# Kernel optimization log

Hardware: AMD Instinct MI355X
Metric: run time of the kernel (lower is better)

## Reference

```python
import jax, jax.numpy as jnp
import numpy as np

TAU = 2.0       # LIF membrane time constant (spikingjelly default)
ALPHA = 2.0     # ATan surrogate sharpness
EPS = 1e-5      # BN eps
NUM_HEADS = 12
PATCH = 2
LENTH = 256     # (H/PATCH)*(W/PATCH)

@jax.custom_vjp
def heaviside(x):
    return (x >= 0.0).astype(x.dtype)

def _hv_fwd(x):
    return heaviside(x), x

def _hv_bwd(x, g):
    sg = ALPHA / 2.0 / (1.0 + (jnp.pi / 2.0 * ALPHA * x) ** 2)  # ATan surrogate
    return (g * sg,)

heaviside.defvjp(_hv_fwd, _hv_bwd)

def lif(x):
    # multi-step LIF over leading time axis, hard reset, v_th = 1.0
    def step(v, xt):
        v = v + (xt - v) / TAU
        s = heaviside(v - 1.0)
        return v * (1.0 - s), s
    _, s = jax.lax.scan(step, jnp.zeros_like(x[0]), x)
    return s

def setup_inputs() -> dict:
    key = jax.random.key(0)
    ks = jax.random.split(key, 9)
    T, B, C, H, W = 4, 4, 384, 32, 32
    x = jax.random.normal(ks[0], (T, B, C, H, W), dtype=jnp.float32)
    Wconv = jax.random.normal(ks[1], (2 * C, C, PATCH, PATCH), dtype=jnp.float32) * (1.0 / np.sqrt(C * PATCH * PATCH))
    gamma1 = jax.random.uniform(ks[2], (2 * C,), dtype=jnp.float32, minval=0.5, maxval=1.5)
    beta1 = jax.random.normal(ks[3], (2 * C,), dtype=jnp.float32) * 0.1
    Wproj = jax.random.normal(ks[4], (C, C), dtype=jnp.float32) * (1.0 / np.sqrt(C))
    gamma2 = jax.random.uniform(ks[5], (C,), dtype=jnp.float32, minval=0.5, maxval=1.5)
    beta2 = jax.random.normal(ks[6], (C,), dtype=jnp.float32) * 0.1
    firing_rate_x = jax.random.uniform(ks[7], (1, 1, NUM_HEADS, 1, 1), dtype=jnp.float32, minval=0.05, maxval=0.5)
    firing_rate_attn = jax.random.uniform(ks[8], (1, 1, NUM_HEADS, 1, 1), dtype=jnp.float32, minval=0.05, maxval=0.5)
    return {"x": x, "Wconv": Wconv, "gamma1": gamma1, "beta1": beta1, "Wproj": Wproj,
            "gamma2": gamma2, "beta2": beta2, "firing_rate_x": firing_rate_x,
            "firing_rate_attn": firing_rate_attn}

def reference(x, Wconv, gamma1, beta1, Wproj, gamma2, beta2, firing_rate_x, firing_rate_attn):
    T, B, C, H, W = x.shape
    d = C // NUM_HEADS
    xs = lif(x)                                          # spikes [T,B,C,H,W]
    # patch conv dim -> 2*dim, stride = kernel = PATCH (eval BN: running mean 0, var 1)
    y = jax.lax.conv_general_dilated(xs.reshape(T * B, C, H, W), Wconv,
                                     (PATCH, PATCH), 'VALID',
                                     dimension_numbers=('NCHW', 'OIHW', 'NCHW'))
    bn1 = gamma1 / jnp.sqrt(1.0 + EPS)
    y = y * bn1[None, :, None, None] + beta1[None, :, None, None]
    Np = (H // PATCH) * (W // PATCH)                     # == LENTH
    y = y.reshape(T, B, NUM_HEADS, 2 * d, Np)
    y1, y2 = y[:, :, :, :d, :], y[:, :, :, d:, :]
    xr = xs.reshape(T, B, NUM_HEADS, d, H * W)
    scale1 = 1.0 / jnp.sqrt(firing_rate_x * d)
    attn = jnp.einsum('tbhdn,tbhdm->tbhnm', y1, xr) * scale1   # [T,B,h,Np,HW]
    attn = lif(attn)
    scale2 = 1.0 / jnp.sqrt(firing_rate_attn * LENTH)
    out = jnp.einsum('tbhdn,tbhnm->tbhdm', y2, attn) * scale2  # [T,B,h,d,HW]
    out = out.reshape(T, B, C, H, W)
    out = lif(out)
    out = jnp.einsum('oc,tbchw->tbohw', Wproj, out)            # 1x1 conv proj
    bn2 = gamma2 / jnp.sqrt(1.0 + EPS)
    out = out * bn2[None, None, :, None, None] + beta2[None, None, :, None, None]
    return out + x
```

## Files before the change

### kernel.cpp

```cpp
#include <hip/hip_runtime.h>
#include <hip/hip_bf16.h>
#include <math.h>


typedef __attribute__((ext_vector_type(8))) short short8;
typedef __attribute__((ext_vector_type(4))) float f32x4;

#define T_ 4
#define B_ 4
#define C_ 384
#define HW 1024
#define NH_ 12
#define Np_ 256
#define EPS_ 1e-5f
#define LDK 56

static __device__ __forceinline__ unsigned short f2bf(float f) {
    __hip_bfloat16 h = __float2bfloat16(f);
    return *reinterpret_cast<unsigned short*>(&h);
}
static __device__ __forceinline__ float bf2f(unsigned short u) {
    __hip_bfloat16 h = *reinterpret_cast<__hip_bfloat16*>(&u);
    return __bfloat162float(h);
}
static __device__ __forceinline__ void split3(float w, unsigned short& u0,
                                              unsigned short& u1, unsigned short& u2) {
    u0 = f2bf(w);  float f0 = bf2f(u0);
    float r1 = w - f0;
    u1 = f2bf(r1); float f1 = bf2f(u1);
    u2 = f2bf(r1 - f1);
}

__global__ __launch_bounds__(256) void k_wsplit(const float* __restrict__ Wc,
                                                const float* __restrict__ Wp,
                                                unsigned short* __restrict__ Wc3,
                                                unsigned short* __restrict__ Wp3) {
    const int NC = 768 * 1536;
    const int NP = 384 * 384;
    int i = blockIdx.x * 256 + threadIdx.x;
    float w; unsigned short* dst; int idx, plane;
    if (i < NC) { w = Wc[i]; dst = Wc3; idx = i; plane = NC; }
    else {
        int j = i - NC;
        if (j >= NP) return;
        w = Wp[j]; dst = Wp3; idx = j; plane = NP;
    }
    unsigned short u0, u1, u2;
    split3(w, u0, u1, u2);
    dst[idx] = u0; dst[plane + idx] = u1; dst[2 * plane + idx] = u2;
}

__global__ __launch_bounds__(256) void k_lif_im2col(const float* __restrict__ x,
                                                    unsigned short* __restrict__ Bc,
                                                    unsigned short* __restrict__ xsb) {
    int gt = blockIdx.x * 256 + threadIdx.x;
    int pw = gt & 15, ph = (gt >> 4) & 15;
    int v = gt >> 8;
    int c = v % 384, b = v / 384;
    float v00 = 0.f, v01 = 0.f, v10 = 0.f, v11 = 0.f;
    const size_t xrow = ((size_t)b * C_ + c) * HW + (size_t)(2 * ph) * 32 + 2 * pw;
#pragma unroll
    for (int t = 0; t < T_; ++t) {
        const float* px = x + (size_t)t * (B_ * C_ * HW) + xrow;
        float2 r0 = *(const float2*)px;
        float2 r1 = *(const float2*)(px + 32);
        v00 += (r0.x - v00) * 0.5f;
        v01 += (r0.y - v01) * 0.5f;
        v10 += (r1.x - v10) * 0.5f;
        v11 += (r1.y - v11) * 0.5f;
        ushort4 s;
        s.x = (v00 >= 1.f) ? 0x3F80 : 0; if (v00 >= 1.f) v00 = 0.f;
        s.y = (v01 >= 1.f) ? 0x3F80 : 0; if (v01 >= 1.f) v01 = 0.f;
        s.z = (v10 >= 1.f) ? 0x3F80 : 0; if (v10 >= 1.f) v10 = 0.f;
        s.w = (v11 >= 1.f) ? 0x3F80 : 0; if (v11 >= 1.f) v11 = 0.f;
        int tb = t * B_ + b;
        int n = tb * 256 + ph * 16 + pw;
        *(ushort4*)(Bc + (size_t)n * 1536 + 4 * c) = s;
        size_t xo = ((size_t)tb * C_ + c) * HW + (size_t)(2 * ph) * 32 + 2 * pw;
        ushort2 w0 = {s.x, s.y}, w1 = {s.z, s.w};
        *(ushort2*)(xsb + xo) = w0;
        *(ushort2*)(xsb + xo + 32) = w1;
    }
}

__global__ __launch_bounds__(256) void k_mconv(const unsigned short* __restrict__ Bc,
                                               const unsigned short* __restrict__ Wc3,
                                               const float* __restrict__ g1,
                                               const float* __restrict__ b1,
                                               const float* __restrict__ frx,
                                               const float* __restrict__ fra,
                                               unsigned short* __restrict__ y1s,
                                               unsigned short* __restrict__ y2s) {
    __shared__ short As[3][64][LDK];
    __shared__ short Bs[128][LDK];
    const int nb = blockIdx.x, mb = blockIdx.y;
    const int tid = threadIdx.x;
    const int lane = tid & 63, wave = tid >> 6;
    const int wm = wave >> 1, wn = wave & 1;
    const int quad = lane >> 4, lr = lane & 15;
    const int arow = tid >> 2, akoff = (tid & 3) * 8;
    f32x4 acc[2][4];
#pragma unroll
    for (int im = 0; im < 2; ++im)
#pragma unroll
        for (int in = 0; in < 4; ++in)
            acc[im][in] = (f32x4){0.f, 0.f, 0.f, 0.f};

    for (int k0 = 0; k0 < 1536; k0 += 32) {
#pragma unroll
        for (int s = 0; s < 3; ++s) {
            short8 a = *(const short8*)(Wc3 + ((size_t)(s * 768 + mb * 64 + arow)) * 1536 + k0 + akoff);
            *(short8*)&As[s][arow][akoff] = a;
        }
#pragma unroll
        for (int i = 0; i < 2; ++i) {
            int f = i * 256 + tid;
            int row = f >> 2, koff = (f & 3) * 8;
            short8 bv = *(const short8*)(Bc + ((size_t)(nb * 128 + row)) * 1536 + k0 + koff);
            *(short8*)&Bs[row][koff] = bv;
        }
        __syncthreads();
        short8 bf[4], af[3][2];
#pragma unroll
        for (int in = 0; in < 4; ++in)
            bf[in] = *(const short8*)&Bs[wn * 64 + in * 16 + lr][quad * 8];
#pragma unroll
        for (int s = 0; s < 3; ++s)
#pragma unroll
            for (int im = 0; im < 2; ++im)
                af[s][im] = *(const short8*)&As[s][wm * 32 + im * 16 + lr][quad * 8];
#pragma unroll
        for (int s = 0; s < 3; ++s)
#pragma unroll
            for (int im = 0; im < 2; ++im)
#pragma unroll
                for (int in = 0; in < 4; ++in)
                    acc[im][in] = __builtin_amdgcn_mfma_f32_16x16x32_bf16(af[s][im], bf[in], acc[im][in], 0, 0, 0);
        __syncthreads();
    }
    const float rs = 1.0f / sqrtf(1.0f + EPS_);
    const int h = mb;
    const float scl = (wm == 0) ? (1.0f / sqrtf(frx[h] * 32.0f))
                                : (1.0f / sqrtf(fra[h] * 256.0f));
    unsigned short* dst = (wm == 0) ? y1s : y2s;
#pragma unroll
    for (int im = 0; im < 2; ++im) {
#pragma unroll
        for (int in = 0; in < 4; ++in) {
            int n_g = nb * 128 + wn * 64 + in * 16 + lr;
            int tb = n_g >> 8, pn = n_g & 255;
            size_t base = (size_t)(tb * NH_ + h) * 3 * 8192;
            ushort4 o0, o1, o2;
#pragma unroll
            for (int r = 0; r < 4; ++r) {
                int oc = mb * 64 + wm * 32 + im * 16 + quad * 4 + r;
                float val = (acc[im][in][r] * (g1[oc] * rs) + b1[oc]) * scl;
                unsigned short u0, u1, u2;
                split3(val, u0, u1, u2);
                ((unsigned short*)&o0)[r] = u0;
                ((unsigned short*)&o1)[r] = u1;
                ((unsigned short*)&o2)[r] = u2;
            }
            int dd = im * 16 + quad * 4;
            if (wm == 0) {
                *(ushort4*)&dst[base + 0 * 8192 + (size_t)pn * 32 + dd] = o0;
                *(ushort4*)&dst[base + 1 * 8192 + (size_t)pn * 32 + dd] = o1;
                *(ushort4*)&dst[base + 2 * 8192 + (size_t)pn * 32 + dd] = o2;
            } else {
#pragma unroll
                for (int r = 0; r < 4; ++r) {
                    dst[base + 0 * 8192 + (size_t)(dd + r) * 256 + pn] = ((unsigned short*)&o0)[r];
                    dst[base + 1 * 8192 + (size_t)(dd + r) * 256 + pn] = ((unsigned short*)&o1)[r];
                    dst[base + 2 * 8192 + (size_t)(dd + r) * 256 + pn] = ((unsigned short*)&o2)[r];
                }
            }
        }
    }
}

__global__ __launch_bounds__(256) void k_attn2(const unsigned short* __restrict__ xsb,
                                               const unsigned short* __restrict__ y1s,
                                               const unsigned short* __restrict__ y2s,
                                               unsigned short* __restrict__ obt) {
    __shared__ unsigned short xb[32][40];
    __shared__ unsigned short pb[32][264];
    const int mt0 = blockIdx.x * 32;
    const int h = blockIdx.y;
    const int b = blockIdx.z;
    const int tid = threadIdx.x;
    const int lane = tid & 63, wv = tid >> 6;
    const int quad = lane >> 4, lr = lane & 15;
    const int dt = wv >> 1, ct = wv & 1;

    float vat[4][2][4];
#pragma unroll
    for (int it = 0; it < 4; ++it)
#pragma unroll
        for (int jt = 0; jt < 2; ++jt)
#pragma unroll
            for (int r = 0; r < 4; ++r) vat[it][jt][r] = 0.f;
    float vo[4] = {0.f, 0.f, 0.f, 0.f};

    for (int t = 0; t < T_; ++t) {
        const int tb = t * B_ + b;
#pragma unroll
        for (int i = 0; i < 4; ++i) {
            int e = tid + i * 256;
            int d = e >> 5, j = e & 31;
            xb[j][d] = xsb[((size_t)tb * C_ + h * 32 + d) * HW + mt0 + j];
        }
        __syncthreads();

        short8 bx[2];
#pragma unroll
        for (int jt = 0; jt < 2; ++jt)
            bx[jt] = *(const short8*)&xb[jt * 16 + lr][quad * 8];

        f32x4 acc[4][2];
#pragma unroll
        for (int it = 0; it < 4; ++it)
#pragma unroll
            for (int jt = 0; jt < 2; ++jt)
                acc[it][jt] = (f32x4){0.f, 0.f, 0.f, 0.f};

        const unsigned short* y1p = y1s + (size_t)(tb * NH_ + h) * 3 * 8192
                                        + (size_t)(wv * 64 + lr) * 32 + quad * 8;
#pragma unroll
        for (int s = 0; s < 3; ++s)
#pragma unroll
            for (int it = 0; it < 4; ++it) {
                short8 a = *(const short8*)(y1p + s * 8192 + it * 512);
#pragma unroll
                for (int jt = 0; jt < 2; ++jt)
                    acc[it][jt] = __builtin_amdgcn_mfma_f32_16x16x32_bf16(a, bx[jt], acc[it][jt], 0, 0, 0);
            }

#pragma unroll
        for (int it = 0; it < 4; ++it)
#pragma unroll
            for (int jt = 0; jt < 2; ++jt) {
                ushort4 sp;
#pragma unroll
                for (int r = 0; r < 4; ++r) {
                    float v = vat[it][jt][r];
                    v += (acc[it][jt][r] - v) * 0.5f;
                    bool s = (v >= 1.0f);
                    ((unsigned short*)&sp)[r] = s ? 0x3F80 : 0;
                    vat[it][jt][r] = s ? 0.f : v;
                }
                *(ushort4*)&pb[jt * 16 + lr][wv * 64 + it * 16 + quad * 4] = sp;
            }
        __syncthreads();

        f32x4 acc2 = (f32x4){0.f, 0.f, 0.f, 0.f};
        const unsigned short* y2p = y2s + (size_t)(tb * NH_ + h) * 3 * 8192
                                        + (size_t)(dt * 16 + lr) * 256 + quad * 8;
#pragma unroll
        for (int s = 0; s < 3; ++s)
#pragma unroll
            for (int k0 = 0; k0 < 256; k0 += 32) {
                short8 a2 = *(const short8*)(y2p + s * 8192 + k0);
                short8 b2 = *(const short8*)&pb[ct * 16 + lr][k0 + quad * 8];
                acc2 = __builtin_amdgcn_mfma_f32_16x16x32_bf16(a2, b2, acc2, 0, 0, 0);
            }

        ushort4 ob;
#pragma unroll
        for (int r = 0; r < 4; ++r) {
            float v = vo[r];
            v += (acc2[r] - v) * 0.5f;
            bool s = (v >= 1.0f);
            ((unsigned short*)&ob)[r] = s ? 0x3F80 : 0;
            vo[r] = s ? 0.f : v;
        }
        *(ushort4*)(obt + ((size_t)tb * HW + mt0 + ct * 16 + lr) * C_
                        + h * 32 + dt * 16 + quad * 4) = ob;
        __syncthreads();
    }
}

__global__ __launch_bounds__(256) void k_mproj(const unsigned short* __restrict__ obt,
                                               const unsigned short* __restrict__ Wp3,
                                               const float* __restrict__ g2,
                                               const float* __restrict__ b2,
                                               const float* __restrict__ x,
                                               float* __restrict__ out) {
    __shared__ short As[3][64][LDK];
    __shared__ short Bs[128][LDK];
    const int nb = blockIdx.x, mb = blockIdx.y;
    const int tid = threadIdx.x;
    const int lane = tid & 63, wave = tid >> 6;
    const int wm = wave >> 1, wn = wave & 1;
    const int quad = lane >> 4, lr = lane & 15;
    const int arow = tid >> 2, akoff = (tid & 3) * 8;
    f32x4 acc[2][4];
#pragma unroll
    for (int im = 0; im < 2; ++im)
#pragma unroll
        for (int in = 0; in < 4; ++in)
            acc[im][in] = (f32x4){0.f, 0.f, 0.f, 0.f};

    for (int k0 = 0; k0 < 384; k0 += 32) {
#pragma unroll
        for (int s = 0; s < 3; ++s) {
            short8 a = *(const short8*)(Wp3 + ((size_t)(s * 384 + mb * 64 + arow)) * 384 + k0 + akoff);
            *(short8*)&As[s][arow][akoff] = a;
        }
#pragma unroll
        for (int i = 0; i < 2; ++i) {
            int f = i * 256 + tid;
            int row = f >> 2, koff = (f & 3) * 8;
            short8 bv = *(const short8*)(obt + ((size_t)(nb * 128 + row)) * 384 + k0 + koff);
            *(short8*)&Bs[row][koff] = bv;
        }
        __syncthreads();
        short8 bf[4], af[3][2];
#pragma unroll
        for (int in = 0; in < 4; ++in)
            bf[in] = *(const short8*)&Bs[wn * 64 + in * 16 + lr][quad * 8];
#pragma unroll
        for (int s = 0; s < 3; ++s)
#pragma unroll
            for (int im = 0; im < 2; ++im)
                af[s][im] = *(const short8*)&As[s][wm * 32 + im * 16 + lr][quad * 8];
#pragma unroll
        for (int s = 0; s < 3; ++s)
#pragma unroll
            for (int im = 0; im < 2; ++im)
#pragma unroll
                for (int in = 0; in < 4; ++in)
                    acc[im][in] = __builtin_amdgcn_mfma_f32_16x16x32_bf16(af[s][im], bf[in], acc[im][in], 0, 0, 0);
        __syncthreads();
    }
    const float rs = 1.0f / sqrtf(1.0f + EPS_);
#pragma unroll
    for (int im = 0; im < 2; ++im) {
#pragma unroll
        for (int in = 0; in < 4; ++in) {
            int n_g = nb * 128 + wn * 64 + in * 16 + lr;
            int tb = n_g >> 10, hw = n_g & 1023;
#pragma unroll
            for (int r = 0; r < 4; ++r) {
                int o = mb * 64 + wm * 32 + im * 16 + quad * 4 + r;
                size_t idx = ((size_t)tb * C_ + o) * HW + hw;
                out[idx] = acc[im][in][r] * (g2[o] * rs) + b2[o] + x[idx];
            }
        }
    }
}

extern "C" void kernel_launch(void* const* d_in, const int* in_sizes, int n_in,
                              void* d_out, int out_size, void* d_ws, size_t ws_size,
                              hipStream_t stream) {
    const float* x      = (const float*)d_in[0];
    const float* Wconv  = (const float*)d_in[1];
    const float* gamma1 = (const float*)d_in[2];
    const float* beta1  = (const float*)d_in[3];
    const float* Wproj  = (const float*)d_in[4];
    const float* gamma2 = (const float*)d_in[5];
    const float* beta2  = (const float*)d_in[6];
    const float* frx    = (const float*)d_in[7];
    const float* fra    = (const float*)d_in[8];
    float* out = (float*)d_out;

    unsigned short* ws16 = (unsigned short*)d_ws;
    unsigned short* Bc  = ws16;
    unsigned short* obt = ws16;
    unsigned short* Wc3 = ws16 + 6291456;
    unsigned short* Wp3 = ws16 + 9830400;
    unsigned short* xsb = ws16 + 10272768;
    unsigned short* y1s = ws16 + 16564224;
    unsigned short* y2s = ws16 + 21282816;

    k_wsplit<<<5184, 256, 0, stream>>>(Wconv, Wproj, Wc3, Wp3);
    k_lif_im2col<<<1536, 256, 0, stream>>>(x, Bc, xsb);
    k_mconv<<<dim3(32, 12), 256, 0, stream>>>(Bc, Wc3, gamma1, beta1, frx, fra, y1s, y2s);
    k_attn2<<<dim3(32, 12, 4), 256, 0, stream>>>(xsb, y1s, y2s, obt);
    k_mproj<<<dim3(128, 6), 256, 0, stream>>>(obt, Wp3, gamma2, beta2, x, out);
}
```

Before: 275.4 us.

## Preload all timesteps of x, double-buffer spike tile, hoist y1/y2 fragment loads

The attention kernel now loads the x tile for all four timesteps into shared memory once at kernel start. It issues every y1 and y2 global fragment load at the top of each timestep, ahead of the MFMAs. The spike tile is double-buffered by timestep parity, so the trailing barrier per timestep is removed. The aim is to hide global-load latency behind MFMA work and cut barrier count. The cost is many more live registers (36 short8 fragments), which could lower occupancy or spill despite the launch bound of 2.

```diff
diff --git a/kernel.cpp b/kernel.cpp
--- a/kernel.cpp
+++ b/kernel.cpp
@@ -178,12 +178,12 @@
     }
 }
 
-__global__ __launch_bounds__(256) void k_attn2(const unsigned short* __restrict__ xsb,
-                                               const unsigned short* __restrict__ y1s,
-                                               const unsigned short* __restrict__ y2s,
-                                               unsigned short* __restrict__ obt) {
-    __shared__ unsigned short xb[32][40];
-    __shared__ unsigned short pb[32][264];
+__global__ __launch_bounds__(256, 2) void k_attn2(const unsigned short* __restrict__ xsb,
+                                                  const unsigned short* __restrict__ y1s,
+                                                  const unsigned short* __restrict__ y2s,
+                                                  unsigned short* __restrict__ obt) {
+    __shared__ unsigned short xb[4][32][40];
+    __shared__ unsigned short pb[2][32][264];
     const int mt0 = blockIdx.x * 32;
     const int h = blockIdx.y;
     const int b = blockIdx.z;
@@ -192,6 +192,14 @@
     const int quad = lane >> 4, lr = lane & 15;
     const int dt = wv >> 1, ct = wv & 1;
 
+#pragma unroll
+    for (int i = 0; i < 16; ++i) {
+        int e = tid + i * 256;
+        int j = e & 31, d = (e >> 5) & 31, t = e >> 10;
+        xb[t][j][d] = xsb[((size_t)((t * B_ + b) * C_) + h * 32 + d) * HW + mt0 + j];
+    }
+    __syncthreads();
+
     float vat[4][2][4];
 #pragma unroll
     for (int it = 0; it < 4; ++it)
@@ -203,18 +211,27 @@
 
     for (int t = 0; t < T_; ++t) {
         const int tb = t * B_ + b;
-#pragma unroll
-        for (int i = 0; i < 4; ++i) {
-            int e = tid + i * 256;
-            int d = e >> 5, j = e & 31;
-            xb[j][d] = xsb[((size_t)tb * C_ + h * 32 + d) * HW + mt0 + j];
-        }
-        __syncthreads();
+        const size_t slab = (size_t)(tb * NH_ + h) * 3 * 8192;
+
+        short8 af[3][4];
+        const unsigned short* y1p = y1s + slab + (size_t)(wv * 64 + lr) * 32 + quad * 8;
+#pragma unroll
+        for (int s = 0; s < 3; ++s)
+#pragma unroll
+            for (int it = 0; it < 4; ++it)
+                af[s][it] = *(const short8*)(y1p + s * 8192 + it * 512);
+        short8 ay[3][8];
+        const unsigned short* y2p = y2s + slab + (size_t)(dt * 16 + lr) * 256 + quad * 8;
+#pragma unroll
+        for (int s = 0; s < 3; ++s)
+#pragma unroll
+            for (int kt = 0; kt < 8; ++kt)
+                ay[s][kt] = *(const short8*)(y2p + s * 8192 + kt * 32);
 
         short8 bx[2];
 #pragma unroll
         for (int jt = 0; jt < 2; ++jt)
-            bx[jt] = *(const short8*)&xb[jt * 16 + lr][quad * 8];
+            bx[jt] = *(const short8*)&xb[t][jt * 16 + lr][quad * 8];
 
         f32x4 acc[4][2];
 #pragma unroll
@@ -222,18 +239,13 @@
 #pragma unroll
             for (int jt = 0; jt < 2; ++jt)
                 acc[it][jt] = (f32x4){0.f, 0.f, 0.f, 0.f};
-
-        const unsigned short* y1p = y1s + (size_t)(tb * NH_ + h) * 3 * 8192
-                                        + (size_t)(wv * 64 + lr) * 32 + quad * 8;
-#pragma unroll
-        for (int s = 0; s < 3; ++s)
-#pragma unroll
-            for (int it = 0; it < 4; ++it) {
-                short8 a = *(const short8*)(y1p + s * 8192 + it * 512);
+#pragma unroll
+        for (int s = 0; s < 3; ++s)
+#pragma unroll
+            for (int it = 0; it < 4; ++it)
 #pragma unroll
                 for (int jt = 0; jt < 2; ++jt)
-                    acc[it][jt] = __builtin_amdgcn_mfma_f32_16x16x32_bf16(a, bx[jt], acc[it][jt], 0, 0, 0);
-            }
+                    acc[it][jt] = __builtin_amdgcn_mfma_f32_16x16x32_bf16(af[s][it], bx[jt], acc[it][jt], 0, 0, 0);
 
 #pragma unroll
         for (int it = 0; it < 4; ++it)
@@ -248,20 +260,17 @@
                     ((unsigned short*)&sp)[r] = s ? 0x3F80 : 0;
                     vat[it][jt][r] = s ? 0.f : v;
                 }
-                *(ushort4*)&pb[jt * 16 + lr][wv * 64 + it * 16 + quad * 4] = sp;
+                *(ushort4*)&pb[t & 1][jt * 16 + lr][wv * 64 + it * 16 + quad * 4] = sp;
             }
         __syncthreads();
 
         f32x4 acc2 = (f32x4){0.f, 0.f, 0.f, 0.f};
-        const unsigned short* y2p = y2s + (size_t)(tb * NH_ + h) * 3 * 8192
-                                        + (size_t)(dt * 16 + lr) * 256 + quad * 8;
-#pragma unroll
-        for (int s = 0; s < 3; ++s)
-#pragma unroll
-            for (int k0 = 0; k0 < 256; k0 += 32) {
-                short8 a2 = *(const short8*)(y2p + s * 8192 + k0);
-                short8 b2 = *(const short8*)&pb[ct * 16 + lr][k0 + quad * 8];
-                acc2 = __builtin_amdgcn_mfma_f32_16x16x32_bf16(a2, b2, acc2, 0, 0, 0);
+#pragma unroll
+        for (int s = 0; s < 3; ++s)
+#pragma unroll
+            for (int kt = 0; kt < 8; ++kt) {
+                short8 b2 = *(const short8*)&pb[t & 1][ct * 16 + lr][kt * 32 + quad * 8];
+                acc2 = __builtin_amdgcn_mfma_f32_16x16x32_bf16(ay[s][kt], b2, acc2, 0, 0, 0);
             }
 
         ushort4 ob;
@@ -275,7 +284,6 @@
         }
         *(ushort4*)(obt + ((size_t)tb * HW + mt0 + ct * 16 + lr) * C_
                         + h * 32 + dt * 16 + quad * 4) = ob;
-        __syncthreads();
     }
 }
 
```

Result: faster. 268.4 us (-2.5%).
